# Kernel tuning notes

Measured on AMD Instinct MI355X. Metric: run time of the kernel, lower is better.

The kernel has to match this reference:

```python
import jax, jax.numpy as jnp
import numpy as np

N, E, D_IN, D_H, L = 50000, 600000, 256, 128, 3


def setup_inputs() -> dict:
    key = jax.random.key(0)
    ks = jax.random.split(key, 10)
    w = lambda k, *sh: jax.random.normal(k, sh, jnp.float32) * 0.05
    z = lambda *sh: jnp.zeros(sh, jnp.float32)
    return {
        "x": jax.random.normal(ks[0], (N, D_IN), jnp.float32),
        "edge_index": jax.random.randint(ks[1], (2, E), 0, N),
        # input projection
        "w_in": w(ks[2], D_IN, D_H), "b_in": z(D_H),
        # stacked GCNConv weights/biases for L layers
        "w_gcn": w(ks[3], L, D_H, D_H), "b_gcn": z(L, D_H),
        # node classifier MLP
        "w_nc1": w(ks[4], D_H, D_H), "b_nc1": z(D_H),
        "w_nc2": w(ks[5], D_H, 1), "b_nc2": z(1),
        # origin classifier MLP
        "w_oc1": w(ks[6], D_H, D_H), "b_oc1": z(D_H),
        "w_oc2": w(ks[7], D_H, 1), "b_oc2": z(1),
    }


def _forward(x, edge_index, w_in, b_in, w_gcn, b_gcn,
             w_nc1, b_nc1, w_nc2, b_nc2, w_oc1, b_oc1, w_oc2, b_oc2):
    # GCNConv default: add self loops, symmetric D^{-1/2} (A+I) D^{-1/2} normalization
    loops = jnp.arange(N)
    row = jnp.concatenate([edge_index[0], loops])  # source nodes
    col = jnp.concatenate([edge_index[1], loops])  # target nodes
    deg = jax.ops.segment_sum(jnp.ones_like(col, x.dtype), col, num_segments=N)
    dinv = jnp.where(deg > 0, jax.lax.rsqrt(deg), 0.0)
    norm = dinv[row] * dinv[col]                   # [E+N]

    h = jax.nn.relu(x @ w_in + b_in)               # [N, D_H]
    for l in range(L):
        xw = h @ w_gcn[l]                          # linear transform first (PyG order)
        agg = jax.ops.segment_sum(xw[row] * norm[:, None], col, num_segments=N)
        h = jax.nn.relu(h + agg + b_gcn[l])        # residual + relu; dropout=identity (eval)

    def mlp_sig(h, w1, b1, w2, b2):
        return jax.nn.sigmoid(jax.nn.relu(h @ w1 + b1) @ w2 + b2)[:, 0]

    node_pred = mlp_sig(h, w_nc1, b_nc1, w_nc2, b_nc2)
    origin_pred = mlp_sig(h, w_oc1, b_oc1, w_oc2, b_oc2)
    error_type_pred = jnp.zeros((N, 4), x.dtype)
    return node_pred, origin_pred, error_type_pred, h


def reference(x, edge_index, w_in, b_in, w_gcn, b_gcn,
              w_nc1, b_nc1, w_nc2, b_nc2, w_oc1, b_oc1, w_oc2, b_oc2):
    return _forward(x, edge_index, w_in, b_in, w_gcn, b_gcn,
                    w_nc1, b_nc1, w_nc2, b_nc2, w_oc1, b_oc1, w_oc2, b_oc2)
```

## Files before the change

### kernel.cpp

```cpp
#include <hip/hip_runtime.h>
#include <math.h>

#define DH 128

typedef short short8 __attribute__((ext_vector_type(8)));
typedef float f32x4 __attribute__((ext_vector_type(4)));

__device__ __forceinline__ unsigned short f2bu(float f) {
  unsigned int u = __builtin_bit_cast(unsigned int, f);
  unsigned int r = (u + 0x7fffu + ((u >> 16) & 1u)) >> 16;
  return (unsigned short)r;
}
__device__ __forceinline__ float blo(unsigned int u) {
  return __builtin_bit_cast(float, u << 16);
}
__device__ __forceinline__ float bhi(unsigned int u) {
  return __builtin_bit_cast(float, u & 0xffff0000u);
}
__device__ __forceinline__ unsigned int packb2(float a, float b) {
  return (unsigned int)f2bu(a) | ((unsigned int)f2bu(b) << 16);
}


__global__ __launch_bounds__(256) void prep_kernel(
    const float* __restrict__ w_in, const float* __restrict__ w_gcn,
    const float* __restrict__ w_nc1, const float* __restrict__ w_oc1,
    unsigned short* __restrict__ w_inT, unsigned short* __restrict__ w_gcnT,
    unsigned short* __restrict__ w_nc1T, unsigned short* __restrict__ w_oc1T,
    int* __restrict__ cnt, float* __restrict__ out_err, int n) {
  int idx = blockIdx.x * 256 + threadIdx.x;
  if (idx < 32768) {
    int k = idx >> 7, c = idx & 127;
    w_inT[c * 256 + k] = f2bu(w_in[idx]);
  } else if (idx < 81920) {
    int sub = idx - 32768;
    int off = sub & 16383;
    int k = off >> 7, c = off & 127;
    w_gcnT[(sub >> 14) * 16384 + c * 128 + k] = f2bu(w_gcn[sub]);
  } else if (idx < 98304) {
    int off = idx - 81920;
    int k = off >> 7, c = off & 127;
    w_nc1T[c * 128 + k] = f2bu(w_nc1[off]);
  } else if (idx < 114688) {
    int off = idx - 98304;
    int k = off >> 7, c = off & 127;
    w_oc1T[c * 128 + k] = f2bu(w_oc1[off]);
  } else if (idx < 114688 + n) {
    cnt[idx - 114688] = 0;
  } else if (idx < 114688 + 5 * n) {
    out_err[idx - 114688 - n] = 0.f;
  }
}


__global__ void count_kernel(const int* __restrict__ col, int* __restrict__ cnt,
                             int* __restrict__ rank, int e) {
  int i = blockIdx.x * blockDim.x + threadIdx.x;
  if (i < e) rank[i] = atomicAdd(&cnt[col[i]], 1);
}

__global__ __launch_bounds__(1024) void scan1_kernel(const int* __restrict__ cnt,
                                                     int* __restrict__ rowptr,
                                                     float* __restrict__ dinv,
                                                     int* __restrict__ bsum, int n) {
  __shared__ int wsum[16];
  const int t = threadIdx.x;
  const int lane = t & 63, wid = t >> 6;
  const int i = blockIdx.x * 1024 + t;
  int v = (i < n) ? cnt[i] : 0;
  int s = v;
#pragma unroll
  for (int d = 1; d < 64; d <<= 1) {
    int u = __shfl_up(s, d);
    if (lane >= d) s += u;
  }
  if (lane == 63) wsum[wid] = s;
  __syncthreads();
  if (t < 16) {
    int ws = wsum[t];
#pragma unroll
    for (int d = 1; d < 16; d <<= 1) {
      int u = __shfl_up(ws, d);
      if (t >= d) ws += u;
    }
    wsum[t] = ws;
  }
  __syncthreads();
  if (i < n) {
    rowptr[i] = (wid ? wsum[wid - 1] : 0) + s - v;
    dinv[i] = rsqrtf((float)(v + 1));
  }
  if (t == 0) bsum[blockIdx.x] = wsum[15];
}

__global__ __launch_bounds__(256) void scan3_kernel(int* __restrict__ rowptr,
                                                    const int* __restrict__ bsum,
                                                    int n, int nb) {
  __shared__ int pre[64];
  int total = 0;
  if (threadIdx.x < 64) {
    int v = (threadIdx.x < nb) ? bsum[threadIdx.x] : 0;
    int s = v;
#pragma unroll
    for (int d = 1; d < 64; d <<= 1) {
      int u = __shfl_up(s, d);
      if ((threadIdx.x & 63) >= d) s += u;
    }
    pre[threadIdx.x] = s - v;
    total = s;
  }
  __syncthreads();
  int i = blockIdx.x * 256 + threadIdx.x;
  if (i < n) rowptr[i] += pre[i >> 10];
  if (blockIdx.x == 0 && threadIdx.x == 63) rowptr[n] = total;
}

__global__ void fill_kernel(const int* __restrict__ row, const int* __restrict__ col,
                            const int* __restrict__ rowptr, const int* __restrict__ rank,
                            int* __restrict__ csr, int e) {
  int i = blockIdx.x * blockDim.x + threadIdx.x;
  if (i < e) csr[rowptr[col[i]] + rank[i]] = row[i];
}


template <int K, bool A_FP32, int MODE>
__global__ __launch_bounds__(256) void gemm_kernel(const void* __restrict__ A_,
                                                   const unsigned short* __restrict__ WT,
                                                   const float* __restrict__ bias,
                                                   const float* __restrict__ dscale,
                                                   float* __restrict__ Cf,
                                                   unsigned short* __restrict__ Cb, int n) {
  const int t = threadIdx.x;
  const int lane = t & 63;
  const int w = t >> 6;
  const int wr = w >> 1, wc = w & 1;
  const int lr = lane & 15, lg = lane >> 4;
  const int r_base = blockIdx.x * 128 + wr * 64;
  const int c_base = wc * 64;

  f32x4 acc[4][4] = {};

#pragma unroll
  for (int kk = 0; kk < K / 32; kk++) {
    const int koff = kk * 32 + lg * 8;
    short8 a[4], b[4];
#pragma unroll
    for (int m = 0; m < 4; m++) {
      int row = r_base + m * 16 + lr;
      row = row < n ? row : n - 1;
      if (A_FP32) {
        const float* Af = (const float*)A_;
        float4 p = *(const float4*)&Af[(size_t)row * K + koff];
        float4 q = *(const float4*)&Af[(size_t)row * K + koff + 4];
        short8 av;
        av[0] = (short)f2bu(p.x); av[1] = (short)f2bu(p.y);
        av[2] = (short)f2bu(p.z); av[3] = (short)f2bu(p.w);
        av[4] = (short)f2bu(q.x); av[5] = (short)f2bu(q.y);
        av[6] = (short)f2bu(q.z); av[7] = (short)f2bu(q.w);
        a[m] = av;
      } else {
        const unsigned short* Ab = (const unsigned short*)A_;
        a[m] = *(const short8*)&Ab[(size_t)row * K + koff];
      }
    }
#pragma unroll
    for (int nb = 0; nb < 4; nb++) {
      int col = c_base + nb * 16 + lr;
      b[nb] = *(const short8*)&WT[(size_t)col * K + koff];
    }
#pragma unroll
    for (int m = 0; m < 4; m++)
#pragma unroll
      for (int nb = 0; nb < 4; nb++)
        acc[m][nb] = __builtin_amdgcn_mfma_f32_16x16x32_bf16(a[m], b[nb], acc[m][nb], 0, 0, 0);
  }

  float bcol[4];
  if (MODE != 0) {
#pragma unroll
    for (int nb = 0; nb < 4; nb++) bcol[nb] = bias[c_base + nb * 16 + lr];
  }

#pragma unroll
  for (int m = 0; m < 4; m++) {
#pragma unroll
    for (int i = 0; i < 4; i++) {
      int row = r_base + m * 16 + lg * 4 + i;
      if (row < n) {
        float sc = (MODE == 0) ? dscale[row] : 0.f;
#pragma unroll
        for (int nb = 0; nb < 4; nb++) {
          int col = c_base + nb * 16 + lr;
          float v = acc[m][nb][i];
          if (MODE == 0) {
            Cb[(size_t)row * DH + col] = f2bu(v * sc);
          } else {
            v = fmaxf(v + bcol[nb], 0.f);
            Cf[(size_t)row * DH + col] = v;
            Cb[(size_t)row * DH + col] = f2bu(v);
          }
        }
      }
    }
  }
}


__global__ __launch_bounds__(256) void agg_kernel(const uint2* __restrict__ xwb2,
                                                  const float* __restrict__ dinv,
                                                  const int* __restrict__ rowptr,
                                                  const int* __restrict__ csr,
                                                  const float* __restrict__ bias,
                                                  float* __restrict__ h,
                                                  uint2* __restrict__ hb2, int n) {
  const int node = blockIdx.x * 4 + (threadIdx.x >> 6);
  if (node >= n) return;
  const int lane = threadIdx.x & 63;
  const int half = lane >> 5;
  const int cidx = lane & 31;
  const float self = dinv[node];

  float a0, a1, a2, a3;
  if (half == 0) {
    uint2 su = xwb2[(size_t)node * 32 + cidx];
    a0 = blo(su.x); a1 = bhi(su.x);
    a2 = blo(su.y); a3 = bhi(su.y);
  } else {
    a0 = a1 = a2 = a3 = 0.f;
  }

  const int beg = rowptr[node], end = rowptr[node + 1];
  int j = beg;
  for (; j + 8 <= end; j += 8) {
    int s0 = csr[j + half], s1 = csr[j + 2 + half];
    int s2 = csr[j + 4 + half], s3 = csr[j + 6 + half];
    uint2 u0 = xwb2[(size_t)s0 * 32 + cidx];
    uint2 u1 = xwb2[(size_t)s1 * 32 + cidx];
    uint2 u2 = xwb2[(size_t)s2 * 32 + cidx];
    uint2 u3 = xwb2[(size_t)s3 * 32 + cidx];
    a0 += blo(u0.x); a1 += bhi(u0.x); a2 += blo(u0.y); a3 += bhi(u0.y);
    a0 += blo(u1.x); a1 += bhi(u1.x); a2 += blo(u1.y); a3 += bhi(u1.y);
    a0 += blo(u2.x); a1 += bhi(u2.x); a2 += blo(u2.y); a3 += bhi(u2.y);
    a0 += blo(u3.x); a1 += bhi(u3.x); a2 += blo(u3.y); a3 += bhi(u3.y);
  }
  for (; j < end; j += 2) {
    int jj = j + half;
    if (jj < end) {
      int s = csr[jj];
      uint2 u = xwb2[(size_t)s * 32 + cidx];
      a0 += blo(u.x); a1 += bhi(u.x); a2 += blo(u.y); a3 += bhi(u.y);
    }
  }

  a0 += __shfl_xor(a0, 32);
  a1 += __shfl_xor(a1, 32);
  a2 += __shfl_xor(a2, 32);
  a3 += __shfl_xor(a3, 32);

  if (half == 0) {
    const float4 bv = *(const float4*)&bias[cidx * 4];
    const float4 hv = *(const float4*)&h[(size_t)node * DH + cidx * 4];
    float r0 = fmaxf(hv.x + self * a0 + bv.x, 0.f);
    float r1 = fmaxf(hv.y + self * a1 + bv.y, 0.f);
    float r2 = fmaxf(hv.z + self * a2 + bv.z, 0.f);
    float r3 = fmaxf(hv.w + self * a3 + bv.w, 0.f);
    *(float4*)&h[(size_t)node * DH + cidx * 4] = make_float4(r0, r1, r2, r3);
    hb2[(size_t)node * 32 + cidx] = make_uint2(packb2(r0, r1), packb2(r2, r3));
  }
}


__global__ __launch_bounds__(256) void heads_kernel(
    const unsigned short* __restrict__ hb,
    const unsigned short* __restrict__ w1T_a, const float* __restrict__ b1_a,
    const float* __restrict__ w2_a, const float* __restrict__ b2_a,
    const unsigned short* __restrict__ w1T_b, const float* __restrict__ b1_b,
    const float* __restrict__ w2_b, const float* __restrict__ b2_b,
    float* __restrict__ out_a, float* __restrict__ out_b, int n) {
  const int t = threadIdx.x;
  const int lane = t & 63;
  const int w = t >> 6;
  const int lr = lane & 15, lg = lane >> 4;
  const int r_base = blockIdx.x * 128 + w * 32;

#pragma unroll
  for (int head = 0; head < 2; head++) {
    const unsigned short* W1T = head ? w1T_b : w1T_a;
    const float* b1 = head ? b1_b : b1_a;
    const float* w2 = head ? w2_b : w2_a;
    const float b2 = head ? b2_b[0] : b2_a[0];
    float* out = head ? out_b : out_a;

    f32x4 acc[2][8] = {};
#pragma unroll
    for (int kk = 0; kk < 4; kk++) {
      const int koff = kk * 32 + lg * 8;
      short8 a[2];
#pragma unroll
      for (int m = 0; m < 2; m++) {
        int row = r_base + m * 16 + lr;
        row = row < n ? row : n - 1;
        a[m] = *(const short8*)&hb[(size_t)row * DH + koff];
      }
#pragma unroll
      for (int nb = 0; nb < 8; nb++) {
        short8 b = *(const short8*)&W1T[(size_t)(nb * 16 + lr) * DH + koff];
#pragma unroll
        for (int m = 0; m < 2; m++)
          acc[m][nb] = __builtin_amdgcn_mfma_f32_16x16x32_bf16(a[m], b, acc[m][nb], 0, 0, 0);
      }
    }

    float b1v[8], w2v[8];
#pragma unroll
    for (int nb = 0; nb < 8; nb++) {
      b1v[nb] = b1[nb * 16 + lr];
      w2v[nb] = w2[nb * 16 + lr];
    }

#pragma unroll
    for (int m = 0; m < 2; m++) {
#pragma unroll
      for (int i = 0; i < 4; i++) {
        float s = 0.f;
#pragma unroll
        for (int nb = 0; nb < 8; nb++)
          s += fmaxf(acc[m][nb][i] + b1v[nb], 0.f) * w2v[nb];
        s += __shfl_xor(s, 1);
        s += __shfl_xor(s, 2);
        s += __shfl_xor(s, 4);
        s += __shfl_xor(s, 8);
        int row = r_base + m * 16 + lg * 4 + i;
        if (lr == 0 && row < n) out[row] = 1.f / (1.f + __expf(-(s + b2)));
      }
    }
  }
}


extern "C" void kernel_launch(void* const* d_in, const int* in_sizes, int n_in,
                              void* d_out, int out_size, void* d_ws, size_t ws_size,
                              hipStream_t stream) {
  const float* x     = (const float*)d_in[0];
  const int*   ei    = (const int*)d_in[1];
  const float* w_in  = (const float*)d_in[2];
  const float* b_in  = (const float*)d_in[3];
  const float* w_gcn = (const float*)d_in[4];
  const float* b_gcn = (const float*)d_in[5];
  const float* w_nc1 = (const float*)d_in[6];
  const float* b_nc1 = (const float*)d_in[7];
  const float* w_nc2 = (const float*)d_in[8];
  const float* b_nc2 = (const float*)d_in[9];
  const float* w_oc1 = (const float*)d_in[10];
  const float* b_oc1 = (const float*)d_in[11];
  const float* w_oc2 = (const float*)d_in[12];
  const float* b_oc2 = (const float*)d_in[13];

  const int N = in_sizes[0] / 256;
  const int E = in_sizes[1] / 2;
  const int* erow = ei;
  const int* ecol = ei + E;

  float* out      = (float*)d_out;
  float* out_node = out;
  float* out_orig = out + N;
  float* out_err  = out + 2 * (size_t)N;
  float* h        = out + 6 * (size_t)N;

  unsigned short* xwb = (unsigned short*)d_ws;
  unsigned short* hb  = xwb + (size_t)N * DH;
  unsigned short* w_inT  = hb + (size_t)N * DH;
  unsigned short* w_gcnT = w_inT + 128 * 256;
  unsigned short* w_nc1T = w_gcnT + 3 * 128 * 128;
  unsigned short* w_oc1T = w_nc1T + 128 * 128;
  float* dinv = (float*)(w_oc1T + 128 * 128);
  int* cnt    = (int*)(dinv + N);
  int* rowptr = cnt + N;
  int* bsum   = rowptr + N + 1;
  int* rank   = bsum + 64;
  int* csr    = rank + E;

  prep_kernel<<<(114688 + 5 * N + 255) / 256, 256, 0, stream>>>(
      w_in, w_gcn, w_nc1, w_oc1, w_inT, w_gcnT, w_nc1T, w_oc1T, cnt, out_err, N);

  const int eb = (E + 255) / 256;
  count_kernel<<<eb, 256, 0, stream>>>(ecol, cnt, rank, E);
  const int nb1 = (N + 1023) / 1024;
  scan1_kernel<<<nb1, 1024, 0, stream>>>(cnt, rowptr, dinv, bsum, N);
  scan3_kernel<<<(N + 255) / 256, 256, 0, stream>>>(rowptr, bsum, N, nb1);
  fill_kernel<<<eb, 256, 0, stream>>>(erow, ecol, rowptr, rank, csr, E);

  const int mb = (N + 127) / 128;
  gemm_kernel<256, true, 1><<<mb, 256, 0, stream>>>(x, w_inT, b_in, nullptr, h, hb, N);
  for (int l = 0; l < 3; l++) {
    gemm_kernel<128, false, 0><<<mb, 256, 0, stream>>>(hb, w_gcnT + (size_t)l * DH * DH,
                                                       nullptr, dinv, nullptr, xwb, N);
    agg_kernel<<<(N + 3) / 4, 256, 0, stream>>>((const uint2*)xwb, dinv, rowptr, csr,
                                                b_gcn + (size_t)l * DH, h,
                                                (uint2*)hb, N);
  }
  heads_kernel<<<mb, 256, 0, stream>>>(hb, w_nc1T, b_nc1, w_nc2, b_nc2,
                                       w_oc1T, b_oc1, w_oc2, b_oc2,
                                       out_node, out_orig, N);
}
```

Before: 258.4 us.

## Halve GEMM row tiles with register double-buffering, unroll gather, fuse head MMAs

The GEMM kernels now handle 64 rows per block instead of 128 and double-buffer the A/B fragment loads in registers, so the next k-slice loads while MFMAs run on the current one. This raises block count and occupancy. The aggregation kernel gets a 16-edge unrolled loop to put more gathers in flight. The heads kernel computes both MLP heads from a single load of each A fragment, at the cost of more blocks and more redundant weight reads per block.

Result: slower. 282.4 us (+9.3%).

```diff
diff --git a/kernel.cpp b/kernel.cpp
--- a/kernel.cpp
+++ b/kernel.cpp
@@ -135,44 +135,52 @@
   const int w = t >> 6;
   const int wr = w >> 1, wc = w & 1;
   const int lr = lane & 15, lg = lane >> 4;
-  const int r_base = blockIdx.x * 128 + wr * 64;
+  const int r_base = blockIdx.x * 64 + wr * 32;
   const int c_base = wc * 64;
-
-  f32x4 acc[4][4] = {};
-
-#pragma unroll
-  for (int kk = 0; kk < K / 32; kk++) {
+  constexpr int NK = K / 32;
+
+  f32x4 acc[2][4] = {};
+  short8 abuf[2][2], bbuf[2][4];
+
+  auto load_ab = [&](int kk, short8(&av)[2], short8(&bv)[4]) {
     const int koff = kk * 32 + lg * 8;
-    short8 a[4], b[4];
-#pragma unroll
-    for (int m = 0; m < 4; m++) {
+#pragma unroll
+    for (int m = 0; m < 2; m++) {
       int row = r_base + m * 16 + lr;
       row = row < n ? row : n - 1;
       if (A_FP32) {
         const float* Af = (const float*)A_;
         float4 p = *(const float4*)&Af[(size_t)row * K + koff];
         float4 q = *(const float4*)&Af[(size_t)row * K + koff + 4];
-        short8 av;
-        av[0] = (short)f2bu(p.x); av[1] = (short)f2bu(p.y);
-        av[2] = (short)f2bu(p.z); av[3] = (short)f2bu(p.w);
-        av[4] = (short)f2bu(q.x); av[5] = (short)f2bu(q.y);
-        av[6] = (short)f2bu(q.z); av[7] = (short)f2bu(q.w);
-        a[m] = av;
+        short8 x;
+        x[0] = (short)f2bu(p.x); x[1] = (short)f2bu(p.y);
+        x[2] = (short)f2bu(p.z); x[3] = (short)f2bu(p.w);
+        x[4] = (short)f2bu(q.x); x[5] = (short)f2bu(q.y);
+        x[6] = (short)f2bu(q.z); x[7] = (short)f2bu(q.w);
+        av[m] = x;
       } else {
         const unsigned short* Ab = (const unsigned short*)A_;
-        a[m] = *(const short8*)&Ab[(size_t)row * K + koff];
+        av[m] = *(const short8*)&Ab[(size_t)row * K + koff];
       }
     }
 #pragma unroll
     for (int nb = 0; nb < 4; nb++) {
       int col = c_base + nb * 16 + lr;
-      b[nb] = *(const short8*)&WT[(size_t)col * K + koff];
-    }
-#pragma unroll
-    for (int m = 0; m < 4; m++)
+      bv[nb] = *(const short8*)&WT[(size_t)col * K + koff];
+    }
+  };
+
+  load_ab(0, abuf[0], bbuf[0]);
+#pragma unroll
+  for (int kk = 0; kk < NK; kk++) {
+    const int cur = kk & 1, nxt = cur ^ 1;
+    if (kk + 1 < NK) load_ab(kk + 1, abuf[nxt], bbuf[nxt]);
+#pragma unroll
+    for (int m = 0; m < 2; m++)
 #pragma unroll
       for (int nb = 0; nb < 4; nb++)
-        acc[m][nb] = __builtin_amdgcn_mfma_f32_16x16x32_bf16(a[m], b[nb], acc[m][nb], 0, 0, 0);
+        acc[m][nb] =
+            __builtin_amdgcn_mfma_f32_16x16x32_bf16(abuf[cur][m], bbuf[cur][nb], acc[m][nb], 0, 0, 0);
   }
 
   float bcol[4];
@@ -182,7 +190,7 @@
   }
 
 #pragma unroll
-  for (int m = 0; m < 4; m++) {
+  for (int m = 0; m < 2; m++) {
 #pragma unroll
     for (int i = 0; i < 4; i++) {
       int row = r_base + m * 16 + lg * 4 + i;
@@ -231,6 +239,19 @@
 
   const int beg = rowptr[node], end = rowptr[node + 1];
   int j = beg;
+  for (; j + 16 <= end; j += 16) {
+    int s[8];
+#pragma unroll
+    for (int k = 0; k < 8; k++) s[k] = csr[j + 2 * k + half];
+    uint2 u[8];
+#pragma unroll
+    for (int k = 0; k < 8; k++) u[k] = xwb2[(size_t)s[k] * 32 + cidx];
+#pragma unroll
+    for (int k = 0; k < 8; k++) {
+      a0 += blo(u[k].x); a1 += bhi(u[k].x);
+      a2 += blo(u[k].y); a3 += bhi(u[k].y);
+    }
+  }
   for (; j + 8 <= end; j += 8) {
     int s0 = csr[j + half], s1 = csr[j + 2 + half];
     int s2 = csr[j + 4 + half], s3 = csr[j + 6 + half];
@@ -281,36 +302,31 @@
   const int lane = t & 63;
   const int w = t >> 6;
   const int lr = lane & 15, lg = lane >> 4;
-  const int r_base = blockIdx.x * 128 + w * 32;
+  const int r_base = blockIdx.x * 64 + w * 16;
+
+  f32x4 acc[2][8] = {};
+#pragma unroll
+  for (int kk = 0; kk < 4; kk++) {
+    const int koff = kk * 32 + lg * 8;
+    int row = r_base + lr;
+    row = row < n ? row : n - 1;
+    short8 a = *(const short8*)&hb[(size_t)row * DH + koff];
+#pragma unroll
+    for (int nb = 0; nb < 8; nb++) {
+      short8 ba = *(const short8*)&w1T_a[(size_t)(nb * 16 + lr) * DH + koff];
+      short8 bb = *(const short8*)&w1T_b[(size_t)(nb * 16 + lr) * DH + koff];
+      acc[0][nb] = __builtin_amdgcn_mfma_f32_16x16x32_bf16(a, ba, acc[0][nb], 0, 0, 0);
+      acc[1][nb] = __builtin_amdgcn_mfma_f32_16x16x32_bf16(a, bb, acc[1][nb], 0, 0, 0);
+    }
+  }
 
 #pragma unroll
   for (int head = 0; head < 2; head++) {
-    const unsigned short* W1T = head ? w1T_b : w1T_a;
     const float* b1 = head ? b1_b : b1_a;
     const float* w2 = head ? w2_b : w2_a;
     const float b2 = head ? b2_b[0] : b2_a[0];
     float* out = head ? out_b : out_a;
 
-    f32x4 acc[2][8] = {};
-#pragma unroll
-    for (int kk = 0; kk < 4; kk++) {
-      const int koff = kk * 32 + lg * 8;
-      short8 a[2];
-#pragma unroll
-      for (int m = 0; m < 2; m++) {
-        int row = r_base + m * 16 + lr;
-        row = row < n ? row : n - 1;
-        a[m] = *(const short8*)&hb[(size_t)row * DH + koff];
-      }
-#pragma unroll
-      for (int nb = 0; nb < 8; nb++) {
-        short8 b = *(const short8*)&W1T[(size_t)(nb * 16 + lr) * DH + koff];
-#pragma unroll
-        for (int m = 0; m < 2; m++)
-          acc[m][nb] = __builtin_amdgcn_mfma_f32_16x16x32_bf16(a[m], b, acc[m][nb], 0, 0, 0);
-      }
-    }
-
     float b1v[8], w2v[8];
 #pragma unroll
     for (int nb = 0; nb < 8; nb++) {
@@ -319,20 +335,17 @@
     }
 
 #pragma unroll
-    for (int m = 0; m < 2; m++) {
-#pragma unroll
-      for (int i = 0; i < 4; i++) {
-        float s = 0.f;
-#pragma unroll
-        for (int nb = 0; nb < 8; nb++)
-          s += fmaxf(acc[m][nb][i] + b1v[nb], 0.f) * w2v[nb];
-        s += __shfl_xor(s, 1);
-        s += __shfl_xor(s, 2);
-        s += __shfl_xor(s, 4);
-        s += __shfl_xor(s, 8);
-        int row = r_base + m * 16 + lg * 4 + i;
-        if (lr == 0 && row < n) out[row] = 1.f / (1.f + __expf(-(s + b2)));
-      }
+    for (int i = 0; i < 4; i++) {
+      float s = 0.f;
+#pragma unroll
+      for (int nb = 0; nb < 8; nb++)
+        s += fmaxf(acc[head][nb][i] + b1v[nb], 0.f) * w2v[nb];
+      s += __shfl_xor(s, 1);
+      s += __shfl_xor(s, 2);
+      s += __shfl_xor(s, 4);
+      s += __shfl_xor(s, 8);
+      int row = r_base + lg * 4 + i;
+      if (lr == 0 && row < n) out[row] = 1.f / (1.f + __expf(-(s + b2)));
     }
   }
 }
@@ -390,7 +403,7 @@
   scan3_kernel<<<(N + 255) / 256, 256, 0, stream>>>(rowptr, bsum, N, nb1);
   fill_kernel<<<eb, 256, 0, stream>>>(erow, ecol, rowptr, rank, csr, E);
 
-  const int mb = (N + 127) / 128;
+  const int mb = (N + 63) / 64;
   gemm_kernel<256, true, 1><<<mb, 256, 0, stream>>>(x, w_inT, b_in, nullptr, h, hb, N);
   for (int l = 0; l < 3; l++) {
     gemm_kernel<128, false, 0><<<mb, 256, 0, stream>>>(hb, w_gcnT + (size_t)l * DH * DH,
```

## Co-schedule CSR build with input and first-layer GEMMs, deepen aggregation unroll

Applied to the files above, without the earlier changes.

The edge counting kernel is merged with the input projection GEMM, and the CSR fill kernel with the first GCN layer GEMM. Each merged kernel splits its grid into a fixed set of grid-stride edge blocks and a set of GEMM tile blocks, so the latency-bound atomic and scatter work overlaps with matrix work and two launches are removed. The aggregation loop also gains a 16-edge unrolled stage that issues eight gathers per half-wave before accumulating, to expose more memory-level parallelism. Costs include fixed block splits that may not balance, and higher register pressure in the aggregation kernel.

After: 239.8 us. -7.2%, faster.

```diff
diff --git a/kernel.cpp b/kernel.cpp
--- a/kernel.cpp
+++ b/kernel.cpp
@@ -53,12 +53,6 @@
 }
 
 
-__global__ void count_kernel(const int* __restrict__ col, int* __restrict__ cnt,
-                             int* __restrict__ rank, int e) {
-  int i = blockIdx.x * blockDim.x + threadIdx.x;
-  if (i < e) rank[i] = atomicAdd(&cnt[col[i]], 1);
-}
-
 __global__ __launch_bounds__(1024) void scan1_kernel(const int* __restrict__ cnt,
                                                      int* __restrict__ rowptr,
                                                      float* __restrict__ dinv,
@@ -115,27 +109,20 @@
   if (blockIdx.x == 0 && threadIdx.x == 63) rowptr[n] = total;
 }
 
-__global__ void fill_kernel(const int* __restrict__ row, const int* __restrict__ col,
-                            const int* __restrict__ rowptr, const int* __restrict__ rank,
-                            int* __restrict__ csr, int e) {
-  int i = blockIdx.x * blockDim.x + threadIdx.x;
-  if (i < e) csr[rowptr[col[i]] + rank[i]] = row[i];
-}
-
 
 template <int K, bool A_FP32, int MODE>
-__global__ __launch_bounds__(256) void gemm_kernel(const void* __restrict__ A_,
-                                                   const unsigned short* __restrict__ WT,
-                                                   const float* __restrict__ bias,
-                                                   const float* __restrict__ dscale,
-                                                   float* __restrict__ Cf,
-                                                   unsigned short* __restrict__ Cb, int n) {
-  const int t = threadIdx.x;
+__device__ __forceinline__ void gemm_tile(const void* __restrict__ A_,
+                                          const unsigned short* __restrict__ WT,
+                                          const float* __restrict__ bias,
+                                          const float* __restrict__ dscale,
+                                          float* __restrict__ Cf,
+                                          unsigned short* __restrict__ Cb, int n,
+                                          int bid, int t) {
   const int lane = t & 63;
   const int w = t >> 6;
   const int wr = w >> 1, wc = w & 1;
   const int lr = lane & 15, lg = lane >> 4;
-  const int r_base = blockIdx.x * 128 + wr * 64;
+  const int r_base = bid * 128 + wr * 64;
   const int c_base = wc * 64;
 
   f32x4 acc[4][4] = {};
@@ -206,6 +193,50 @@
 }
 
 
+__global__ __launch_bounds__(256) void count_ingemm_kernel(
+    const int* __restrict__ ecol, int* __restrict__ cnt, int* __restrict__ rank, int e,
+    const float* __restrict__ x, const unsigned short* __restrict__ w_inT,
+    const float* __restrict__ b_in, float* __restrict__ h,
+    unsigned short* __restrict__ hb, int n, int CB) {
+  if ((int)blockIdx.x < CB) {
+    const int stride = CB * 256;
+    for (int i = blockIdx.x * 256 + threadIdx.x; i < e; i += stride)
+      rank[i] = atomicAdd(&cnt[ecol[i]], 1);
+  } else {
+    gemm_tile<256, true, 1>(x, w_inT, b_in, nullptr, h, hb, n,
+                            blockIdx.x - CB, threadIdx.x);
+  }
+}
+
+
+__global__ __launch_bounds__(256) void fill_gemm_kernel(
+    const int* __restrict__ row, const int* __restrict__ col,
+    const int* __restrict__ rowptr, const int* __restrict__ rank,
+    int* __restrict__ csr, int e,
+    const unsigned short* __restrict__ hb, const unsigned short* __restrict__ wT,
+    const float* __restrict__ dscale, unsigned short* __restrict__ xwb, int n, int FB) {
+  if ((int)blockIdx.x < FB) {
+    const int stride = FB * 256;
+    for (int i = blockIdx.x * 256 + threadIdx.x; i < e; i += stride)
+      csr[rowptr[col[i]] + rank[i]] = row[i];
+  } else {
+    gemm_tile<128, false, 0>(hb, wT, nullptr, dscale, nullptr, xwb, n,
+                             blockIdx.x - FB, threadIdx.x);
+  }
+}
+
+
+template <int K, bool A_FP32, int MODE>
+__global__ __launch_bounds__(256) void gemm_kernel(const void* __restrict__ A_,
+                                                   const unsigned short* __restrict__ WT,
+                                                   const float* __restrict__ bias,
+                                                   const float* __restrict__ dscale,
+                                                   float* __restrict__ Cf,
+                                                   unsigned short* __restrict__ Cb, int n) {
+  gemm_tile<K, A_FP32, MODE>(A_, WT, bias, dscale, Cf, Cb, n, blockIdx.x, threadIdx.x);
+}
+
+
 __global__ __launch_bounds__(256) void agg_kernel(const uint2* __restrict__ xwb2,
                                                   const float* __restrict__ dinv,
                                                   const int* __restrict__ rowptr,
@@ -231,6 +262,19 @@
 
   const int beg = rowptr[node], end = rowptr[node + 1];
   int j = beg;
+  for (; j + 16 <= end; j += 16) {
+    int s[8];
+#pragma unroll
+    for (int k = 0; k < 8; k++) s[k] = csr[j + 2 * k + half];
+    uint2 u[8];
+#pragma unroll
+    for (int k = 0; k < 8; k++) u[k] = xwb2[(size_t)s[k] * 32 + cidx];
+#pragma unroll
+    for (int k = 0; k < 8; k++) {
+      a0 += blo(u[k].x); a1 += bhi(u[k].x);
+      a2 += blo(u[k].y); a3 += bhi(u[k].y);
+    }
+  }
   for (; j + 8 <= end; j += 8) {
     int s0 = csr[j + half], s1 = csr[j + 2 + half];
     int s2 = csr[j + 4 + half], s3 = csr[j + 6 + half];
@@ -383,23 +427,29 @@
   prep_kernel<<<(114688 + 5 * N + 255) / 256, 256, 0, stream>>>(
       w_in, w_gcn, w_nc1, w_oc1, w_inT, w_gcnT, w_nc1T, w_oc1T, cnt, out_err, N);
 
-  const int eb = (E + 255) / 256;
-  count_kernel<<<eb, 256, 0, stream>>>(ecol, cnt, rank, E);
+  const int gb = (N + 127) / 128;
+  const int CB = 160, FB = 160;
+
+  count_ingemm_kernel<<<CB + gb, 256, 0, stream>>>(ecol, cnt, rank, E,
+                                                   x, w_inT, b_in, h, hb, N, CB);
+
   const int nb1 = (N + 1023) / 1024;
   scan1_kernel<<<nb1, 1024, 0, stream>>>(cnt, rowptr, dinv, bsum, N);
   scan3_kernel<<<(N + 255) / 256, 256, 0, stream>>>(rowptr, bsum, N, nb1);
-  fill_kernel<<<eb, 256, 0, stream>>>(erow, ecol, rowptr, rank, csr, E);
-
-  const int mb = (N + 127) / 128;
-  gemm_kernel<256, true, 1><<<mb, 256, 0, stream>>>(x, w_inT, b_in, nullptr, h, hb, N);
-  for (int l = 0; l < 3; l++) {
-    gemm_kernel<128, false, 0><<<mb, 256, 0, stream>>>(hb, w_gcnT + (size_t)l * DH * DH,
+
+  fill_gemm_kernel<<<FB + gb, 256, 0, stream>>>(erow, ecol, rowptr, rank, csr, E,
+                                                hb, w_gcnT, dinv, xwb, N, FB);
+  agg_kernel<<<(N + 3) / 4, 256, 0, stream>>>((const uint2*)xwb, dinv, rowptr, csr,
+                                              b_gcn, h, (uint2*)hb, N);
+
+  for (int l = 1; l < 3; l++) {
+    gemm_kernel<128, false, 0><<<gb, 256, 0, stream>>>(hb, w_gcnT + (size_t)l * DH * DH,
                                                        nullptr, dinv, nullptr, xwb, N);
     agg_kernel<<<(N + 3) / 4, 256, 0, stream>>>((const uint2*)xwb, dinv, rowptr, csr,
                                                 b_gcn + (size_t)l * DH, h,
                                                 (uint2*)hb, N);
   }
-  heads_kernel<<<mb, 256, 0, stream>>>(hb, w_nc1T, b_nc1, w_nc2, b_nc2,
+  heads_kernel<<<gb, 256, 0, stream>>>(hb, w_nc1T, b_nc1, w_nc2, b_nc2,
                                        w_oc1T, b_oc1, w_oc2, b_oc2,
                                        out_node, out_orig, N);
 }
```

## Replace CSR build with fixed-cap ELL and fuse aggregation into per-layer GEMM

Applied to the files above, without the earlier changes.

Replaces the count/scan/fill CSR construction with a single atomic pass that writes neighbours into a fixed-capacity (64) ELL table. That pass runs in the same launch as the input-projection GEMM. Each GCN layer becomes one kernel that first aggregates the normalized bf16 neighbour features and then runs the 128x128 MFMA, which drops the separate xw buffer and agg pass and recomputes dinv from counts. The risks are silent truncation or out-of-bounds writes for nodes with in-degree above 64, nondeterministic neighbour order, and a residual now read from bf16 instead of fp32 h.

Result: no change. 260.9 us (+0.9%).

```diff
diff --git a/kernel.cpp b/kernel.cpp
--- a/kernel.cpp
+++ b/kernel.cpp
@@ -2,6 +2,7 @@
 #include <math.h>
 
 #define DH 128
+#define ELLCAP 64
 
 typedef short short8 __attribute__((ext_vector_type(8)));
 typedef float f32x4 __attribute__((ext_vector_type(4)));
@@ -16,6 +17,9 @@
 }
 __device__ __forceinline__ float bhi(unsigned int u) {
   return __builtin_bit_cast(float, u & 0xffff0000u);
+}
+__device__ __forceinline__ float b2f(unsigned short v) {
+  return __builtin_bit_cast(float, (unsigned int)v << 16);
 }
 __device__ __forceinline__ unsigned int packb2(float a, float b) {
   return (unsigned int)f2bu(a) | ((unsigned int)f2bu(b) << 16);
@@ -53,90 +57,18 @@
 }
 
 
-__global__ void count_kernel(const int* __restrict__ col, int* __restrict__ cnt,
-                             int* __restrict__ rank, int e) {
-  int i = blockIdx.x * blockDim.x + threadIdx.x;
-  if (i < e) rank[i] = atomicAdd(&cnt[col[i]], 1);
-}
-
-__global__ __launch_bounds__(1024) void scan1_kernel(const int* __restrict__ cnt,
-                                                     int* __restrict__ rowptr,
-                                                     float* __restrict__ dinv,
-                                                     int* __restrict__ bsum, int n) {
-  __shared__ int wsum[16];
-  const int t = threadIdx.x;
-  const int lane = t & 63, wid = t >> 6;
-  const int i = blockIdx.x * 1024 + t;
-  int v = (i < n) ? cnt[i] : 0;
-  int s = v;
-#pragma unroll
-  for (int d = 1; d < 64; d <<= 1) {
-    int u = __shfl_up(s, d);
-    if (lane >= d) s += u;
-  }
-  if (lane == 63) wsum[wid] = s;
-  __syncthreads();
-  if (t < 16) {
-    int ws = wsum[t];
-#pragma unroll
-    for (int d = 1; d < 16; d <<= 1) {
-      int u = __shfl_up(ws, d);
-      if (t >= d) ws += u;
-    }
-    wsum[t] = ws;
-  }
-  __syncthreads();
-  if (i < n) {
-    rowptr[i] = (wid ? wsum[wid - 1] : 0) + s - v;
-    dinv[i] = rsqrtf((float)(v + 1));
-  }
-  if (t == 0) bsum[blockIdx.x] = wsum[15];
-}
-
-__global__ __launch_bounds__(256) void scan3_kernel(int* __restrict__ rowptr,
-                                                    const int* __restrict__ bsum,
-                                                    int n, int nb) {
-  __shared__ int pre[64];
-  int total = 0;
-  if (threadIdx.x < 64) {
-    int v = (threadIdx.x < nb) ? bsum[threadIdx.x] : 0;
-    int s = v;
-#pragma unroll
-    for (int d = 1; d < 64; d <<= 1) {
-      int u = __shfl_up(s, d);
-      if ((threadIdx.x & 63) >= d) s += u;
-    }
-    pre[threadIdx.x] = s - v;
-    total = s;
-  }
-  __syncthreads();
-  int i = blockIdx.x * 256 + threadIdx.x;
-  if (i < n) rowptr[i] += pre[i >> 10];
-  if (blockIdx.x == 0 && threadIdx.x == 63) rowptr[n] = total;
-}
-
-__global__ void fill_kernel(const int* __restrict__ row, const int* __restrict__ col,
-                            const int* __restrict__ rowptr, const int* __restrict__ rank,
-                            int* __restrict__ csr, int e) {
-  int i = blockIdx.x * blockDim.x + threadIdx.x;
-  if (i < e) csr[rowptr[col[i]] + rank[i]] = row[i];
-}
-
-
-template <int K, bool A_FP32, int MODE>
-__global__ __launch_bounds__(256) void gemm_kernel(const void* __restrict__ A_,
-                                                   const unsigned short* __restrict__ WT,
-                                                   const float* __restrict__ bias,
-                                                   const float* __restrict__ dscale,
-                                                   float* __restrict__ Cf,
-                                                   unsigned short* __restrict__ Cb, int n) {
-  const int t = threadIdx.x;
+__device__ __forceinline__ void ingemm_tile(const float* __restrict__ A,
+                                            const unsigned short* __restrict__ WT,
+                                            const float* __restrict__ bias,
+                                            unsigned short* __restrict__ Cb, int n,
+                                            int bid, int t) {
   const int lane = t & 63;
   const int w = t >> 6;
   const int wr = w >> 1, wc = w & 1;
   const int lr = lane & 15, lg = lane >> 4;
-  const int r_base = blockIdx.x * 128 + wr * 64;
+  const int r_base = bid * 128 + wr * 64;
   const int c_base = wc * 64;
+  constexpr int K = 256;
 
   f32x4 acc[4][4] = {};
 
@@ -148,20 +80,14 @@
     for (int m = 0; m < 4; m++) {
       int row = r_base + m * 16 + lr;
       row = row < n ? row : n - 1;
-      if (A_FP32) {
-        const float* Af = (const float*)A_;
-        float4 p = *(const float4*)&Af[(size_t)row * K + koff];
-        float4 q = *(const float4*)&Af[(size_t)row * K + koff + 4];
-        short8 av;
-        av[0] = (short)f2bu(p.x); av[1] = (short)f2bu(p.y);
-        av[2] = (short)f2bu(p.z); av[3] = (short)f2bu(p.w);
-        av[4] = (short)f2bu(q.x); av[5] = (short)f2bu(q.y);
-        av[6] = (short)f2bu(q.z); av[7] = (short)f2bu(q.w);
-        a[m] = av;
-      } else {
-        const unsigned short* Ab = (const unsigned short*)A_;
-        a[m] = *(const short8*)&Ab[(size_t)row * K + koff];
-      }
+      float4 p = *(const float4*)&A[(size_t)row * K + koff];
+      float4 q = *(const float4*)&A[(size_t)row * K + koff + 4];
+      short8 av;
+      av[0] = (short)f2bu(p.x); av[1] = (short)f2bu(p.y);
+      av[2] = (short)f2bu(p.z); av[3] = (short)f2bu(p.w);
+      av[4] = (short)f2bu(q.x); av[5] = (short)f2bu(q.y);
+      av[6] = (short)f2bu(q.z); av[7] = (short)f2bu(q.w);
+      a[m] = av;
     }
 #pragma unroll
     for (int nb = 0; nb < 4; nb++) {
@@ -176,10 +102,8 @@
   }
 
   float bcol[4];
-  if (MODE != 0) {
-#pragma unroll
-    for (int nb = 0; nb < 4; nb++) bcol[nb] = bias[c_base + nb * 16 + lr];
-  }
+#pragma unroll
+  for (int nb = 0; nb < 4; nb++) bcol[nb] = bias[c_base + nb * 16 + lr];
 
 #pragma unroll
   for (int m = 0; m < 4; m++) {
@@ -187,18 +111,11 @@
     for (int i = 0; i < 4; i++) {
       int row = r_base + m * 16 + lg * 4 + i;
       if (row < n) {
-        float sc = (MODE == 0) ? dscale[row] : 0.f;
 #pragma unroll
         for (int nb = 0; nb < 4; nb++) {
           int col = c_base + nb * 16 + lr;
-          float v = acc[m][nb][i];
-          if (MODE == 0) {
-            Cb[(size_t)row * DH + col] = f2bu(v * sc);
-          } else {
-            v = fmaxf(v + bcol[nb], 0.f);
-            Cf[(size_t)row * DH + col] = v;
-            Cb[(size_t)row * DH + col] = f2bu(v);
-          }
+          float v = fmaxf(acc[m][nb][i] + bcol[nb], 0.f);
+          Cb[(size_t)row * DH + col] = f2bu(v);
         }
       }
     }
@@ -206,66 +123,135 @@
 }
 
 
-__global__ __launch_bounds__(256) void agg_kernel(const uint2* __restrict__ xwb2,
-                                                  const float* __restrict__ dinv,
-                                                  const int* __restrict__ rowptr,
-                                                  const int* __restrict__ csr,
-                                                  const float* __restrict__ bias,
-                                                  float* __restrict__ h,
-                                                  uint2* __restrict__ hb2, int n) {
-  const int node = blockIdx.x * 4 + (threadIdx.x >> 6);
-  if (node >= n) return;
-  const int lane = threadIdx.x & 63;
-  const int half = lane >> 5;
-  const int cidx = lane & 31;
-  const float self = dinv[node];
-
-  float a0, a1, a2, a3;
-  if (half == 0) {
-    uint2 su = xwb2[(size_t)node * 32 + cidx];
-    a0 = blo(su.x); a1 = bhi(su.x);
-    a2 = blo(su.y); a3 = bhi(su.y);
+__global__ __launch_bounds__(256) void count_ingemm_kernel(
+    const int* __restrict__ erow, const int* __restrict__ ecol,
+    int* __restrict__ cnt, int* __restrict__ ell, int e,
+    const float* __restrict__ x, const unsigned short* __restrict__ w_inT,
+    const float* __restrict__ b_in, unsigned short* __restrict__ hb, int n, int CB) {
+  if ((int)blockIdx.x < CB) {
+    const int stride = CB * 256;
+    for (int i = blockIdx.x * 256 + threadIdx.x; i < e; i += stride) {
+      int c = ecol[i];
+      int pos = atomicAdd(&cnt[c], 1);
+      ell[(size_t)c * ELLCAP + pos] = erow[i];
+    }
   } else {
-    a0 = a1 = a2 = a3 = 0.f;
-  }
-
-  const int beg = rowptr[node], end = rowptr[node + 1];
-  int j = beg;
-  for (; j + 8 <= end; j += 8) {
-    int s0 = csr[j + half], s1 = csr[j + 2 + half];
-    int s2 = csr[j + 4 + half], s3 = csr[j + 6 + half];
-    uint2 u0 = xwb2[(size_t)s0 * 32 + cidx];
-    uint2 u1 = xwb2[(size_t)s1 * 32 + cidx];
-    uint2 u2 = xwb2[(size_t)s2 * 32 + cidx];
-    uint2 u3 = xwb2[(size_t)s3 * 32 + cidx];
-    a0 += blo(u0.x); a1 += bhi(u0.x); a2 += blo(u0.y); a3 += bhi(u0.y);
-    a0 += blo(u1.x); a1 += bhi(u1.x); a2 += blo(u1.y); a3 += bhi(u1.y);
-    a0 += blo(u2.x); a1 += bhi(u2.x); a2 += blo(u2.y); a3 += bhi(u2.y);
-    a0 += blo(u3.x); a1 += bhi(u3.x); a2 += blo(u3.y); a3 += bhi(u3.y);
-  }
-  for (; j < end; j += 2) {
-    int jj = j + half;
-    if (jj < end) {
-      int s = csr[jj];
-      uint2 u = xwb2[(size_t)s * 32 + cidx];
-      a0 += blo(u.x); a1 += bhi(u.x); a2 += blo(u.y); a3 += bhi(u.y);
-    }
-  }
-
-  a0 += __shfl_xor(a0, 32);
-  a1 += __shfl_xor(a1, 32);
-  a2 += __shfl_xor(a2, 32);
-  a3 += __shfl_xor(a3, 32);
-
-  if (half == 0) {
-    const float4 bv = *(const float4*)&bias[cidx * 4];
-    const float4 hv = *(const float4*)&h[(size_t)node * DH + cidx * 4];
-    float r0 = fmaxf(hv.x + self * a0 + bv.x, 0.f);
-    float r1 = fmaxf(hv.y + self * a1 + bv.y, 0.f);
-    float r2 = fmaxf(hv.z + self * a2 + bv.z, 0.f);
-    float r3 = fmaxf(hv.w + self * a3 + bv.w, 0.f);
-    *(float4*)&h[(size_t)node * DH + cidx * 4] = make_float4(r0, r1, r2, r3);
-    hb2[(size_t)node * 32 + cidx] = make_uint2(packb2(r0, r1), packb2(r2, r3));
+    ingemm_tile(x, w_inT, b_in, hb, n, blockIdx.x - CB, threadIdx.x);
+  }
+}
+
+
+__global__ __launch_bounds__(256) void layer_kernel(
+    const unsigned short* __restrict__ hin,
+    const unsigned short* __restrict__ wT,
+    const int* __restrict__ cnt, const int* __restrict__ ell,
+    const float* __restrict__ bias,
+    unsigned short* __restrict__ hout, float* __restrict__ hf, int n) {
+  const int t = threadIdx.x;
+  const int lane = t & 63;
+  const int w = t >> 6;
+  const int lr = lane & 15, lg = lane >> 4;
+  const int r0 = (blockIdx.x * 4 + w) * 16;
+  if (r0 >= n) return;
+  int node = r0 + lr;
+  node = node < n ? node : n - 1;
+
+  const int deg = cnt[node];
+  const float self = rsqrtf((float)(deg + 1));
+  const int ko = lg * 8;
+
+  float g[4][8];
+  {
+    const unsigned short* hrow = hin + (size_t)node * DH;
+#pragma unroll
+    for (int kk = 0; kk < 4; kk++) {
+      uint4 q = *(const uint4*)&hrow[kk * 32 + ko];
+#pragma unroll
+      for (int e2 = 0; e2 < 4; e2++) {
+        unsigned int u = ((const unsigned int*)&q)[e2];
+        g[kk][2 * e2]     = self * blo(u);
+        g[kk][2 * e2 + 1] = self * bhi(u);
+      }
+    }
+  }
+
+  const int* el = ell + (size_t)node * ELLCAP;
+  int j = 0;
+  for (; j + 2 <= deg; j += 2) {
+    int s0 = el[j], s1 = el[j + 1];
+    float w0 = rsqrtf((float)(cnt[s0] + 1));
+    float w1 = rsqrtf((float)(cnt[s1] + 1));
+    const unsigned short* p0 = hin + (size_t)s0 * DH;
+    const unsigned short* p1 = hin + (size_t)s1 * DH;
+    uint4 q0[4], q1[4];
+#pragma unroll
+    for (int kk = 0; kk < 4; kk++) q0[kk] = *(const uint4*)&p0[kk * 32 + ko];
+#pragma unroll
+    for (int kk = 0; kk < 4; kk++) q1[kk] = *(const uint4*)&p1[kk * 32 + ko];
+#pragma unroll
+    for (int kk = 0; kk < 4; kk++) {
+#pragma unroll
+      for (int e2 = 0; e2 < 4; e2++) {
+        unsigned int u0 = ((const unsigned int*)&q0[kk])[e2];
+        unsigned int u1 = ((const unsigned int*)&q1[kk])[e2];
+        g[kk][2 * e2]     = fmaf(w0, blo(u0), fmaf(w1, blo(u1), g[kk][2 * e2]));
+        g[kk][2 * e2 + 1] = fmaf(w0, bhi(u0), fmaf(w1, bhi(u1), g[kk][2 * e2 + 1]));
+      }
+    }
+  }
+  if (j < deg) {
+    int s0 = el[j];
+    float w0 = rsqrtf((float)(cnt[s0] + 1));
+    const unsigned short* p0 = hin + (size_t)s0 * DH;
+#pragma unroll
+    for (int kk = 0; kk < 4; kk++) {
+      uint4 q0 = *(const uint4*)&p0[kk * 32 + ko];
+#pragma unroll
+      for (int e2 = 0; e2 < 4; e2++) {
+        unsigned int u0 = ((const unsigned int*)&q0)[e2];
+        g[kk][2 * e2]     = fmaf(w0, blo(u0), g[kk][2 * e2]);
+        g[kk][2 * e2 + 1] = fmaf(w0, bhi(u0), g[kk][2 * e2 + 1]);
+      }
+    }
+  }
+
+  short8 a[4];
+#pragma unroll
+  for (int kk = 0; kk < 4; kk++) {
+    union { unsigned int u[4]; short8 s; } cv;
+#pragma unroll
+    for (int e2 = 0; e2 < 4; e2++)
+      cv.u[e2] = packb2(self * g[kk][2 * e2], self * g[kk][2 * e2 + 1]);
+    a[kk] = cv.s;
+  }
+
+  f32x4 acc[8] = {};
+#pragma unroll
+  for (int kk = 0; kk < 4; kk++) {
+#pragma unroll
+    for (int nb = 0; nb < 8; nb++) {
+      short8 b = *(const short8*)&wT[(size_t)(nb * 16 + lr) * DH + kk * 32 + ko];
+      acc[nb] = __builtin_amdgcn_mfma_f32_16x16x32_bf16(a[kk], b, acc[nb], 0, 0, 0);
+    }
+  }
+
+  float bcol[8];
+#pragma unroll
+  for (int nb = 0; nb < 8; nb++) bcol[nb] = bias[nb * 16 + lr];
+
+#pragma unroll
+  for (int i = 0; i < 4; i++) {
+    int row = r0 + lg * 4 + i;
+    if (row < n) {
+#pragma unroll
+      for (int nb = 0; nb < 8; nb++) {
+        int col = nb * 16 + lr;
+        float res = b2f(hin[(size_t)row * DH + col]);
+        float v = fmaxf(res + acc[nb][i] + bcol[nb], 0.f);
+        hout[(size_t)row * DH + col] = f2bu(v);
+        if (hf) hf[(size_t)row * DH + col] = v;
+      }
+    }
   }
 }
 
@@ -367,39 +353,32 @@
   float* out_err  = out + 2 * (size_t)N;
   float* h        = out + 6 * (size_t)N;
 
-  unsigned short* xwb = (unsigned short*)d_ws;
-  unsigned short* hb  = xwb + (size_t)N * DH;
-  unsigned short* w_inT  = hb + (size_t)N * DH;
+  unsigned short* hbA = (unsigned short*)d_ws;
+  unsigned short* hbB = hbA + (size_t)N * DH;
+  unsigned short* w_inT  = hbB + (size_t)N * DH;
   unsigned short* w_gcnT = w_inT + 128 * 256;
   unsigned short* w_nc1T = w_gcnT + 3 * 128 * 128;
   unsigned short* w_oc1T = w_nc1T + 128 * 128;
-  float* dinv = (float*)(w_oc1T + 128 * 128);
-  int* cnt    = (int*)(dinv + N);
-  int* rowptr = cnt + N;
-  int* bsum   = rowptr + N + 1;
-  int* rank   = bsum + 64;
-  int* csr    = rank + E;
+  int* cnt = (int*)(w_oc1T + 128 * 128);
+  int* ell = cnt + N;
 
   prep_kernel<<<(114688 + 5 * N + 255) / 256, 256, 0, stream>>>(
       w_in, w_gcn, w_nc1, w_oc1, w_inT, w_gcnT, w_nc1T, w_oc1T, cnt, out_err, N);
 
-  const int eb = (E + 255) / 256;
-  count_kernel<<<eb, 256, 0, stream>>>(ecol, cnt, rank, E);
-  const int nb1 = (N + 1023) / 1024;
-  scan1_kernel<<<nb1, 1024, 0, stream>>>(cnt, rowptr, dinv, bsum, N);
-  scan3_kernel<<<(N + 255) / 256, 256, 0, stream>>>(rowptr, bsum, N, nb1);
-  fill_kernel<<<eb, 256, 0, stream>>>(erow, ecol, rowptr, rank, csr, E);
-
-  const int mb = (N + 127) / 128;
-  gemm_kernel<256, true, 1><<<mb, 256, 0, stream>>>(x, w_inT, b_in, nullptr, h, hb, N);
-  for (int l = 0; l < 3; l++) {
-    gemm_kernel<128, false, 0><<<mb, 256, 0, stream>>>(hb, w_gcnT + (size_t)l * DH * DH,
-                                                       nullptr, dinv, nullptr, xwb, N);
-    agg_kernel<<<(N + 3) / 4, 256, 0, stream>>>((const uint2*)xwb, dinv, rowptr, csr,
-                                                b_gcn + (size_t)l * DH, h,
-                                                (uint2*)hb, N);
-  }
-  heads_kernel<<<mb, 256, 0, stream>>>(hb, w_nc1T, b_nc1, w_nc2, b_nc2,
+  const int gb = (N + 127) / 128;
+  const int CB = 160;
+
+  count_ingemm_kernel<<<CB + gb, 256, 0, stream>>>(erow, ecol, cnt, ell, E,
+                                                   x, w_inT, b_in, hbA, N, CB);
+
+  const int lb = (N + 63) / 64;
+  layer_kernel<<<lb, 256, 0, stream>>>(hbA, w_gcnT, cnt, ell, b_gcn, hbB, nullptr, N);
+  layer_kernel<<<lb, 256, 0, stream>>>(hbB, w_gcnT + 16384, cnt, ell,
+                                       b_gcn + DH, hbA, nullptr, N);
+  layer_kernel<<<lb, 256, 0, stream>>>(hbA, w_gcnT + 32768, cnt, ell,
+                                       b_gcn + 2 * DH, hbB, h, N);
+
+  heads_kernel<<<gb, 256, 0, stream>>>(hbB, w_nc1T, b_nc1, w_nc2, b_nc2,
                                        w_oc1T, b_oc1, w_oc2, b_oc2,
                                        out_node, out_orig, N);
 }
```
